# Kernel optimization log

Measured on AMD Instinct MI355X. Metric: run time of the kernel, lower is better.

## Reference

```python
import jax, jax.numpy as jnp
import numpy as np

B, L, E, H, A = 32, 4096, 512, 512, 256


def setup_inputs() -> dict:
    key = jax.random.key(0)
    ks = jax.random.split(key, 8)
    s_e = 1.0 / np.sqrt(E)
    s_h = 1.0 / np.sqrt(H)
    s_a = 1.0 / np.sqrt(A)
    return {
        "features": jax.random.normal(ks[0], (B, L, E), jnp.float32),
        "decoder_hidden": jax.random.normal(ks[1], (B, H), jnp.float32),
        "W_enc": jax.random.uniform(ks[2], (E, A), jnp.float32, -s_e, s_e),
        "b_enc": jax.random.uniform(ks[3], (A,), jnp.float32, -s_e, s_e),
        "W_dec": jax.random.uniform(ks[4], (H, A), jnp.float32, -s_h, s_h),
        "b_dec": jax.random.uniform(ks[5], (A,), jnp.float32, -s_h, s_h),
        "W_v": jax.random.uniform(ks[6], (A, 1), jnp.float32, -s_a, s_a),
        "b_v": jax.random.uniform(ks[7], (1,), jnp.float32, -s_a, s_a),
    }


def reference(features, decoder_hidden, W_enc, b_enc, W_dec, b_dec, W_v, b_v):
    # encoder/decoder projections
    enc_attn = jnp.einsum("ble,ea->bla", features, W_enc) + b_enc  # [B,L,A]
    dec_attn = decoder_hidden @ W_dec + b_dec                       # [B,A]
    sim = jax.nn.relu(enc_attn + dec_attn[:, None, :])              # [B,L,A]
    scores = (jnp.einsum("bla,ao->blo", sim, W_v) + b_v)[..., 0]    # [B,L]
    attn_weights = jax.nn.softmax(scores, axis=1)                   # [B,L]
    output = jnp.einsum("ble,bl->be", features, attn_weights)       # [B,E]
    return output, attn_weights
```

## Files before the change

kernel.cpp:

```cpp
#include <hip/hip_runtime.h>
#include <hip/hip_bf16.h>
#include <stdint.h>


typedef __attribute__((ext_vector_type(8))) short bf16x8;
typedef __attribute__((ext_vector_type(4))) float f32x4;

__device__ __forceinline__ unsigned short f32_to_bf16(float f) {
    union { float f; unsigned u; } v; v.f = f;
    unsigned u = v.u;
    u += 0x7fffu + ((u >> 16) & 1u);
    return (unsigned short)(u >> 16);
}

__device__ __forceinline__ void async_load16(const void* g, void* l) {
    __builtin_amdgcn_global_load_lds(
        (const __attribute__((address_space(1))) unsigned int*)g,
        (__attribute__((address_space(3))) unsigned int*)l, 16, 0, 0);
}

__global__ __launch_bounds__(256) void prep_kernel(
    const float* __restrict__ dh, const float* __restrict__ W_enc,
    const float* __restrict__ b_enc, const float* __restrict__ W_dec,
    const float* __restrict__ b_dec, unsigned short* __restrict__ Wp,
    float* __restrict__ dec_full)
{
    int t = threadIdx.x;
    if (blockIdx.x < 32) {
        int b = blockIdx.x;
        float a0 = 0.f, a1 = 0.f, a2 = 0.f, a3 = 0.f;
        #pragma unroll 2
        for (int h = 0; h < 512; h += 4) {
            a0 += dh[b * 512 + h + 0] * W_dec[(h + 0) * 256 + t];
            a1 += dh[b * 512 + h + 1] * W_dec[(h + 1) * 256 + t];
            a2 += dh[b * 512 + h + 2] * W_dec[(h + 2) * 256 + t];
            a3 += dh[b * 512 + h + 3] * W_dec[(h + 3) * 256 + t];
        }
        dec_full[b * 256 + t] = (a0 + a1) + (a2 + a3) + b_enc[t] + b_dec[t];
    } else {
        int tid = (blockIdx.x - 32) * 256 + t;
        #pragma unroll
        for (int i = 0; i < 8; ++i) {
            int d = tid + i * 16384;
            int j = d & 7;
            int n = (d >> 3) & 255;
            int chunk = (d >> 11) & 7;
            int kb = d >> 14;
            int k = kb * 64 + chunk * 8 + j;
            Wp[d] = f32_to_bf16(W_enc[k * 256 + n]);
        }
    }
}

union SMemU {
    struct { unsigned short A[8192]; unsigned short B[16384]; } g;
    struct { float red[8][64]; float sblk[128]; float wexp[128];
             float part[4][512]; float mshr; } e;
};

__global__ __launch_bounds__(512, 4) void score_kernel(
    const float* __restrict__ feat, const unsigned short* __restrict__ Wp,
    const float* __restrict__ dec_full, const float* __restrict__ W_v,
    float* __restrict__ scores, float* __restrict__ m_c,
    float* __restrict__ o_part)
{
    __shared__ SMemU sm;

    const int t = threadIdx.x;
    const int lane = t & 63;
    const int wave = t >> 6;
    const int mrow = wave >> 2;
    const int wcol = wave & 3;
    const int r0 = blockIdx.x * 128;
    const int b = blockIdx.x >> 5;

    float wv[4], dec[4];
    #pragma unroll
    for (int ct = 0; ct < 4; ++ct) {
        int a = wcol * 64 + ct * 16 + (lane & 15);
        wv[ct] = W_v[a];
        dec[ct] = dec_full[b * 256 + a];
    }

    f32x4 acc[4][4];
    #pragma unroll
    for (int mt = 0; mt < 4; ++mt)
        #pragma unroll
        for (int ct = 0; ct < 4; ++ct)
            acc[mt][ct] = f32x4{0.f, 0.f, 0.f, 0.f};

    for (int ks = 0; ks < 8; ++ks) {
        #pragma unroll
        for (int q = 0; q < 4; ++q) {
            int c = q * 512 + t;
            async_load16(Wp + ks * 16384 + c * 8, sm.g.B + c * 8);
        }
        #pragma unroll
        for (int it = 0; it < 4; ++it) {
            int lin = it * 512 + t;
            int m = lin >> 4, kq = lin & 15;
            float4 a = *(const float4*)(feat + (size_t)(r0 + m) * 512 + ks * 64 + kq * 4);
            ushort4 w;
            w.x = f32_to_bf16(a.x);
            w.y = f32_to_bf16(a.y);
            w.z = f32_to_bf16(a.z);
            w.w = f32_to_bf16(a.w);
            int chunk = kq >> 1, jh = kq & 1;
            *(ushort4*)(sm.g.A + m * 64 + ((chunk ^ (m & 7)) * 8) + jh * 4) = w;
        }
        __syncthreads();
        #pragma unroll
        for (int kk = 0; kk < 2; ++kk) {
            int chunk = kk * 4 + (lane >> 4);
            bf16x8 bfr[4];
            #pragma unroll
            for (int ct = 0; ct < 4; ++ct) {
                int n = wcol * 64 + ct * 16 + (lane & 15);
                bfr[ct] = *(const bf16x8*)(sm.g.B + (chunk * 256 + n) * 8);
            }
            #pragma unroll
            for (int mt = 0; mt < 4; ++mt) {
                int m = mrow * 64 + mt * 16 + (lane & 15);
                bf16x8 afr = *(const bf16x8*)(sm.g.A + m * 64 + ((chunk ^ (m & 7)) * 8));
                #pragma unroll
                for (int ct = 0; ct < 4; ++ct)
                    acc[mt][ct] = __builtin_amdgcn_mfma_f32_16x16x32_bf16(
                        afr, bfr[ct], acc[mt][ct], 0, 0, 0);
            }
        }
        __syncthreads();
    }

    #pragma unroll
    for (int mt = 0; mt < 4; ++mt) {
        #pragma unroll
        for (int r = 0; r < 4; ++r) {
            float p = 0.f;
            #pragma unroll
            for (int ct = 0; ct < 4; ++ct) {
                float v = acc[mt][ct][r] + dec[ct];
                v = v > 0.f ? v : 0.f;
                p += v * wv[ct];
            }
            p += __shfl_xor(p, 1);
            p += __shfl_xor(p, 2);
            p += __shfl_xor(p, 4);
            p += __shfl_xor(p, 8);
            if ((lane & 15) == 0)
                sm.e.red[wave][mt * 16 + (lane >> 4) * 4 + r] = p;
        }
    }
    __syncthreads();
    if (t < 128) {
        int mr = t >> 6, u = t & 63;
        float v = sm.e.red[mr * 4 + 0][u] + sm.e.red[mr * 4 + 1][u]
                + sm.e.red[mr * 4 + 2][u] + sm.e.red[mr * 4 + 3][u];
        sm.e.sblk[t] = v;
        scores[r0 + t] = v;
    }
    __syncthreads();
    if (t < 64) {
        float m = fmaxf(sm.e.sblk[t], sm.e.sblk[t + 64]);
        #pragma unroll
        for (int o = 1; o < 64; o <<= 1) m = fmaxf(m, __shfl_xor(m, o));
        if (t == 0) sm.e.mshr = m;
    }
    __syncthreads();
    float mb = sm.e.mshr;
    if (t < 128) sm.e.wexp[t] = __expf(sm.e.sblk[t] - mb);
    __syncthreads();

    int e4 = t & 127, g = t >> 7;
    float ax = 0.f, ay = 0.f, az = 0.f, aw = 0.f;
    #pragma unroll 8
    for (int i = 0; i < 32; ++i) {
        int l = g * 32 + i;
        float wl = sm.e.wexp[l];
        const float4 f = *(const float4*)(feat + (size_t)(r0 + l) * 512 + e4 * 4);
        ax += wl * f.x; ay += wl * f.y; az += wl * f.z; aw += wl * f.w;
    }
    if (g) {
        float4 w; w.x = ax; w.y = ay; w.z = az; w.w = aw;
        *(float4*)&sm.e.part[g][e4 * 4] = w;
    }
    __syncthreads();
    if (g == 0) {
        const float4 p1 = *(const float4*)&sm.e.part[1][e4 * 4];
        const float4 p2 = *(const float4*)&sm.e.part[2][e4 * 4];
        const float4 p3 = *(const float4*)&sm.e.part[3][e4 * 4];
        float4 r;
        r.x = ax + p1.x + p2.x + p3.x;
        r.y = ay + p1.y + p2.y + p3.y;
        r.z = az + p1.z + p2.z + p3.z;
        r.w = aw + p1.w + p2.w + p3.w;
        *(float4*)(o_part + (size_t)blockIdx.x * 512 + e4 * 4) = r;
        if (t == 0) m_c[blockIdx.x] = mb;
    }
}

__global__ __launch_bounds__(256) void softmax_kernel(
    const float* __restrict__ scores, float* __restrict__ out,
    float* __restrict__ MZ)
{
    __shared__ float sred[4];
    __shared__ float zred[4];
    int b = blockIdx.x, t = threadIdx.x;

    const float* s = scores + b * 4096;
    float vals[16];
    float m = -1e30f;
    #pragma unroll
    for (int i = 0; i < 16; ++i) { vals[i] = s[t + i * 256]; m = fmaxf(m, vals[i]); }
    #pragma unroll
    for (int o = 1; o < 64; o <<= 1) m = fmaxf(m, __shfl_xor(m, o));
    if ((t & 63) == 0) sred[t >> 6] = m;
    __syncthreads();
    m = fmaxf(fmaxf(sred[0], sred[1]), fmaxf(sred[2], sred[3]));

    float z = 0.f;
    #pragma unroll
    for (int i = 0; i < 16; ++i) { vals[i] = __expf(vals[i] - m); z += vals[i]; }
    #pragma unroll
    for (int o = 1; o < 64; o <<= 1) z += __shfl_xor(z, o);
    if ((t & 63) == 0) zred[t >> 6] = z;
    __syncthreads();
    z = zred[0] + zred[1] + zred[2] + zred[3];
    float inv = 1.f / z;
    #pragma unroll
    for (int i = 0; i < 16; ++i)
        out[16384 + b * 4096 + t + i * 256] = vals[i] * inv;
    if (t == 0) { MZ[b] = m; MZ[32 + b] = z; }
}

__global__ __launch_bounds__(256) void combine_kernel(
    const float* __restrict__ o_part, const float* __restrict__ m_c,
    const float* __restrict__ MZ, float* __restrict__ out)
{
    __shared__ float sc[32];
    int b = blockIdx.x, t = threadIdx.x;
    if (t < 32) sc[t] = __expf(m_c[b * 32 + t] - MZ[b]) * (1.f / MZ[32 + b]);
    __syncthreads();
    float a0 = 0.f, a1 = 0.f;
    #pragma unroll 8
    for (int c = 0; c < 32; ++c) {
        const float2 v = *(const float2*)(o_part + (size_t)(b * 32 + c) * 512 + t * 2);
        a0 += sc[c] * v.x; a1 += sc[c] * v.y;
    }
    float2 r; r.x = a0; r.y = a1;
    *(float2*)(out + b * 512 + t * 2) = r;
}

extern "C" void kernel_launch(void* const* d_in, const int* in_sizes, int n_in,
                              void* d_out, int out_size, void* d_ws, size_t ws_size,
                              hipStream_t stream) {
    const float* feat  = (const float*)d_in[0];
    const float* dh    = (const float*)d_in[1];
    const float* W_enc = (const float*)d_in[2];
    const float* b_enc = (const float*)d_in[3];
    const float* W_dec = (const float*)d_in[4];
    const float* b_dec = (const float*)d_in[5];
    const float* W_v   = (const float*)d_in[6];

    unsigned short* Wp = (unsigned short*)d_ws;
    float* dec_full = (float*)((char*)d_ws + 262144);
    float* scores   = (float*)((char*)d_ws + 294912);
    float* m_c      = (float*)((char*)d_ws + 819200);
    float* MZ       = (float*)((char*)d_ws + 823296);
    float* o_part   = (float*)((char*)d_ws + 1048576);
    float* out      = (float*)d_out;

    prep_kernel<<<96, 256, 0, stream>>>(dh, W_enc, b_enc, W_dec, b_dec, Wp, dec_full);
    score_kernel<<<1024, 512, 0, stream>>>(feat, Wp, dec_full, W_v, scores, m_c, o_part);
    softmax_kernel<<<32, 256, 0, stream>>>(scores, out, MZ);
    combine_kernel<<<32, 256, 0, stream>>>(o_part, m_c, MZ, out);
}
```

Baseline: 456.1 us.

## Double-buffer async LDS staging of features and weights in score kernel

The score GEMM loop now stages raw fp32 feature tiles and bf16 weight tiles into two alternating LDS buffers with async global-to-LDS loads. The next K-slice is prefetched while MFMAs run on the current one, and only one barrier per iteration is needed. The K-step is halved to 32 and the weight packing in the prep kernel is changed to match. Feature conversion to bf16 moves from the global-load path to after the LDS read. In exchange, per-block LDS grows, which may lower occupancy, and the unswizzled fp32 A tile may cause LDS bank conflicts.

```diff
diff --git a/kernel.cpp b/kernel.cpp
--- a/kernel.cpp
+++ b/kernel.cpp
@@ -44,16 +44,16 @@
             int d = tid + i * 16384;
             int j = d & 7;
             int n = (d >> 3) & 255;
-            int chunk = (d >> 11) & 7;
-            int kb = d >> 14;
-            int k = kb * 64 + chunk * 8 + j;
+            int chunk = (d >> 11) & 3;
+            int kb = d >> 13;
+            int k = kb * 32 + chunk * 8 + j;
             Wp[d] = f32_to_bf16(W_enc[k * 256 + n]);
         }
     }
 }
 
 union SMemU {
-    struct { unsigned short A[8192]; unsigned short B[16384]; } g;
+    struct { float A[2][4096]; unsigned short B[2][8192]; } g;
     struct { float red[8][64]; float sblk[128]; float wexp[128];
              float part[4][512]; float mshr; } e;
 };
@@ -89,47 +89,60 @@
         for (int ct = 0; ct < 4; ++ct)
             acc[mt][ct] = f32x4{0.f, 0.f, 0.f, 0.f};
 
-    for (int ks = 0; ks < 8; ++ks) {
-        #pragma unroll
-        for (int q = 0; q < 4; ++q) {
-            int c = q * 512 + t;
-            async_load16(Wp + ks * 16384 + c * 8, sm.g.B + c * 8);
-        }
-        #pragma unroll
-        for (int it = 0; it < 4; ++it) {
-            int lin = it * 512 + t;
-            int m = lin >> 4, kq = lin & 15;
-            float4 a = *(const float4*)(feat + (size_t)(r0 + m) * 512 + ks * 64 + kq * 4);
-            ushort4 w;
-            w.x = f32_to_bf16(a.x);
-            w.y = f32_to_bf16(a.y);
-            w.z = f32_to_bf16(a.z);
-            w.w = f32_to_bf16(a.w);
-            int chunk = kq >> 1, jh = kq & 1;
-            *(ushort4*)(sm.g.A + m * 64 + ((chunk ^ (m & 7)) * 8) + jh * 4) = w;
-        }
+    #define STAGE(ks_, buf_)                                                     \
+        do {                                                                     \
+            _Pragma("unroll")                                                    \
+            for (int i = 0; i < 2; ++i) {                                        \
+                int cell = i * 512 + t;                                          \
+                int m_ = cell >> 3, kq_ = cell & 7;                              \
+                async_load16(feat + (size_t)(r0 + m_) * 512 + (ks_) * 32 + kq_ * 4, \
+                             &sm.g.A[buf_][cell * 4]);                           \
+            }                                                                    \
+            _Pragma("unroll")                                                    \
+            for (int i = 0; i < 2; ++i) {                                        \
+                int cell = i * 512 + t;                                          \
+                async_load16(Wp + (ks_) * 8192 + cell * 8,                       \
+                             &sm.g.B[buf_][cell * 8]);                           \
+            }                                                                    \
+        } while (0)
+
+    STAGE(0, 0);
+
+    const int q = lane >> 4;
+    const int c = lane & 15;
+
+    for (int ks = 0; ks < 16; ++ks) {
+        const int buf = ks & 1;
         __syncthreads();
-        #pragma unroll
-        for (int kk = 0; kk < 2; ++kk) {
-            int chunk = kk * 4 + (lane >> 4);
-            bf16x8 bfr[4];
+        if (ks < 15) STAGE(ks + 1, buf ^ 1);
+
+        bf16x8 bfr[4];
+        #pragma unroll
+        for (int ct = 0; ct < 4; ++ct) {
+            int n = wcol * 64 + ct * 16 + c;
+            bfr[ct] = *(const bf16x8*)(&sm.g.B[buf][(q * 256 + n) * 8]);
+        }
+        #pragma unroll
+        for (int mt = 0; mt < 4; ++mt) {
+            int m = mrow * 64 + mt * 16 + c;
+            const float4 lo = *(const float4*)(&sm.g.A[buf][m * 32 + q * 8]);
+            const float4 hi = *(const float4*)(&sm.g.A[buf][m * 32 + q * 8 + 4]);
+            bf16x8 afr;
+            afr[0] = (short)f32_to_bf16(lo.x);
+            afr[1] = (short)f32_to_bf16(lo.y);
+            afr[2] = (short)f32_to_bf16(lo.z);
+            afr[3] = (short)f32_to_bf16(lo.w);
+            afr[4] = (short)f32_to_bf16(hi.x);
+            afr[5] = (short)f32_to_bf16(hi.y);
+            afr[6] = (short)f32_to_bf16(hi.z);
+            afr[7] = (short)f32_to_bf16(hi.w);
             #pragma unroll
-            for (int ct = 0; ct < 4; ++ct) {
-                int n = wcol * 64 + ct * 16 + (lane & 15);
-                bfr[ct] = *(const bf16x8*)(sm.g.B + (chunk * 256 + n) * 8);
-            }
-            #pragma unroll
-            for (int mt = 0; mt < 4; ++mt) {
-                int m = mrow * 64 + mt * 16 + (lane & 15);
-                bf16x8 afr = *(const bf16x8*)(sm.g.A + m * 64 + ((chunk ^ (m & 7)) * 8));
-                #pragma unroll
-                for (int ct = 0; ct < 4; ++ct)
-                    acc[mt][ct] = __builtin_amdgcn_mfma_f32_16x16x32_bf16(
-                        afr, bfr[ct], acc[mt][ct], 0, 0, 0);
-            }
-        }
-        __syncthreads();
-    }
+            for (int ct = 0; ct < 4; ++ct)
+                acc[mt][ct] = __builtin_amdgcn_mfma_f32_16x16x32_bf16(
+                    afr, bfr[ct], acc[mt][ct], 0, 0, 0);
+        }
+    }
+    __syncthreads();
 
     #pragma unroll
     for (int mt = 0; mt < 4; ++mt) {
@@ -196,6 +209,7 @@
         *(float4*)(o_part + (size_t)blockIdx.x * 512 + e4 * 4) = r;
         if (t == 0) m_c[blockIdx.x] = mb;
     }
+    #undef STAGE
 }
 
 __global__ __launch_bounds__(256) void softmax_kernel(
```

After: 607.2 us. 33.1% more time.
